# Kernel tuning notes

Measured on AMD Instinct MI355X. Metric: run time of the kernel, lower is better.

Reference implementation:

```python
import jax, jax.numpy as jnp
import numpy as np

V = 50257       # vocab size (leaves of Huffman tree)
N_DEC = V - 1   # internal decision nodes
D = 1024        # input_size
N_EX = 8192     # number of examples (tokens)
MAX_LEN = 24    # max Huffman path depth


def setup_inputs() -> dict:
    key = jax.random.key(0)
    k_x, k_w, k_t, k_p, k_c, k_l = jax.random.split(key, 6)
    x = jax.random.normal(k_x, (N_EX, D), dtype=jnp.float32)
    W = jax.random.normal(k_w, (N_DEC, D), dtype=jnp.float32) * 0.02
    t = jax.random.randint(k_t, (N_EX,), 0, V, dtype=jnp.int32)
    # padded per-leaf tree paths: decision-node indices and +/-1 branch codes
    paths = jax.random.randint(k_p, (V, MAX_LEN), 0, N_DEC, dtype=jnp.int32)
    codes = jnp.where(jax.random.bernoulli(k_c, 0.5, (V, MAX_LEN)), 1.0, -1.0).astype(jnp.float32)
    lens = jax.random.randint(k_l, (V,), 1, MAX_LEN + 1, dtype=jnp.int32)
    return {"x": x, "W": W, "t": t, "paths": paths, "codes": codes, "lens": lens}


def reference(x, W, t, paths, codes, lens):
    # Per-example tree path: gather the decision nodes / codes for each target leaf.
    node_idx = paths[t]            # [N_EX, MAX_LEN] int32
    code = codes[t]                # [N_EX, MAX_LEN] +/-1
    mask = (jnp.arange(MAX_LEN)[None, :] < lens[t][:, None]).astype(x.dtype)  # [N_EX, MAX_LEN]
    # Irregular gather of W rows along each path, then per-step dot products.
    Wp = W[node_idx]               # [N_EX, MAX_LEN, D]
    wxy = code * jnp.einsum('nd,nld->nl', x, Wp)   # [N_EX, MAX_LEN]
    # Per-decision binary log-loss: log(1 + exp(-wxy)), masked to true path length.
    ls = jax.nn.softplus(-wxy) * mask
    return ls.sum()
```

## Files before the change

kernel.cpp:

```cpp
#include <hip/hip_runtime.h>
#include <math.h>

#define HS_D       1024
#define HS_MAXLEN  24
#define HS_PAIRS   12
#define HS_NBUCKET 512

__global__ __launch_bounds__(256) void hsm_pair_kernel(
    const float* __restrict__ x,
    const float* __restrict__ W,
    const int*   __restrict__ t,
    const int*   __restrict__ paths,
    const float* __restrict__ codes,
    const int*   __restrict__ lens,
    float*       __restrict__ ws,
    int n_ex)
{
    const int tid  = threadIdx.x;
    const int lane = tid & 63;
    const int gw   = blockIdx.x * 4 + (tid >> 6);
    const int n    = gw / HS_PAIRS;
    const int p    = gw % HS_PAIRS;

    const int leaf = t[n];
    const int L    = lens[leaf];
    const int l0   = 2 * p;
    const int l1   = l0 + 1;
    if (l0 >= L) return;

    const int   node0 = paths[leaf * HS_MAXLEN + l0];
    const float c0    = codes[leaf * HS_MAXLEN + l0];
    const bool  v1    = (l1 < L);
    const int   node1 = v1 ? paths[leaf * HS_MAXLEN + l1] : node0;
    const float c1    = v1 ? codes[leaf * HS_MAXLEN + l1] : 1.0f;

    const float4* x4 = (const float4*)(x + (size_t)n     * HS_D);
    const float4* w0 = (const float4*)(W + (size_t)node0 * HS_D);
    const float4* w1 = (const float4*)(W + (size_t)node1 * HS_D);

    float4 xf[4], wf0[4], wf1[4];
#pragma unroll
    for (int j = 0; j < 4; ++j) xf[j]  = x4[j * 64 + lane];
#pragma unroll
    for (int j = 0; j < 4; ++j) wf0[j] = w0[j * 64 + lane];
#pragma unroll
    for (int j = 0; j < 4; ++j) wf1[j] = w1[j * 64 + lane];

    float d0 = 0.0f, d1 = 0.0f;
#pragma unroll
    for (int j = 0; j < 4; ++j) {
        d0 += xf[j].x * wf0[j].x + xf[j].y * wf0[j].y
            + xf[j].z * wf0[j].z + xf[j].w * wf0[j].w;
        d1 += xf[j].x * wf1[j].x + xf[j].y * wf1[j].y
            + xf[j].z * wf1[j].z + xf[j].w * wf1[j].w;
    }

#pragma unroll
    for (int off = 32; off > 0; off >>= 1) {
        d0 += __shfl_down(d0, off);
        d1 += __shfl_down(d1, off);
    }

    if (lane == 0) {
        const float z0 = -c0 * d0;
        float v = fmaxf(z0, 0.0f) + log1pf(expf(-fabsf(z0)));
        if (v1) {
            const float z1 = -c1 * d1;
            v += fmaxf(z1, 0.0f) + log1pf(expf(-fabsf(z1)));
        }
        atomicAdd(&ws[gw & (HS_NBUCKET - 1)], v);
    }
}

__global__ __launch_bounds__(64) void hsm_finish_kernel(
    const float* __restrict__ ws, float* __restrict__ out)
{
    const int lane = threadIdx.x;
    float s = 0.0f;
#pragma unroll
    for (int k = 0; k < HS_NBUCKET / 64; ++k)
        s += ws[lane + 64 * k];
#pragma unroll
    for (int off = 32; off > 0; off >>= 1)
        s += __shfl_down(s, off);
    if (lane == 0) out[0] = s;
}

extern "C" void kernel_launch(void* const* d_in, const int* in_sizes, int n_in,
                              void* d_out, int out_size, void* d_ws, size_t ws_size,
                              hipStream_t stream) {
    const float* x     = (const float*)d_in[0];
    const float* W     = (const float*)d_in[1];
    const int*   t     = (const int*)  d_in[2];
    const int*   paths = (const int*)  d_in[3];
    const float* codes = (const float*)d_in[4];
    const int*   lens  = (const int*)  d_in[5];
    float* out = (float*)d_out;
    float* ws  = (float*)d_ws;

    const int n_ex = in_sizes[2];

    hipMemsetAsync(ws, 0, HS_NBUCKET * sizeof(float), stream);

    const int n_waves  = n_ex * HS_PAIRS;
    const int n_blocks = (n_waves + 3) / 4;
    hsm_pair_kernel<<<n_blocks, 256, 0, stream>>>(x, W, t, paths, codes, lens,
                                                  ws, n_ex);
    hsm_finish_kernel<<<1, 64, 0, stream>>>(ws, out);
}
```

Baseline: 324.2 us.

## Warm L2/MALL with a streaming prefetch pass and drop atomic bucket reduction

```diff
diff --git a/kernel.cpp b/kernel.cpp
--- a/kernel.cpp
+++ b/kernel.cpp
@@ -4,7 +4,26 @@
 #define HS_D       1024
 #define HS_MAXLEN  24
 #define HS_PAIRS   12
-#define HS_NBUCKET 512
+#define HS_PF_OFF  (1u << 21)
+
+__global__ __launch_bounds__(256) void hsm_prefetch_kernel(
+    const float4* __restrict__ W4, int nW4,
+    const float4* __restrict__ x4, int nx4,
+    float* __restrict__ ws)
+{
+    const int tid    = blockIdx.x * blockDim.x + threadIdx.x;
+    const int stride = gridDim.x * blockDim.x;
+    float s = 0.0f;
+    for (int i = tid; i < nW4; i += stride) {
+        const float4 v = W4[i];
+        s += v.x + v.y + v.z + v.w;
+    }
+    for (int i = tid; i < nx4; i += stride) {
+        const float4 v = x4[i];
+        s += v.x + v.y + v.z + v.w;
+    }
+    ws[HS_PF_OFF + tid] = s;
+}
 
 __global__ __launch_bounds__(256) void hsm_pair_kernel(
     const float* __restrict__ x,
@@ -13,8 +32,7 @@
     const int*   __restrict__ paths,
     const float* __restrict__ codes,
     const int*   __restrict__ lens,
-    float*       __restrict__ ws,
-    int n_ex)
+    float*       __restrict__ ws)
 {
     const int tid  = threadIdx.x;
     const int lane = tid & 63;
@@ -26,7 +44,10 @@
     const int L    = lens[leaf];
     const int l0   = 2 * p;
     const int l1   = l0 + 1;
-    if (l0 >= L) return;
+    if (l0 >= L) {
+        if (lane == 0) ws[gw] = 0.0f;
+        return;
+    }
 
     const int   node0 = paths[leaf * HS_MAXLEN + l0];
     const float c0    = codes[leaf * HS_MAXLEN + l0];
@@ -34,17 +55,17 @@
     const int   node1 = v1 ? paths[leaf * HS_MAXLEN + l1] : node0;
     const float c1    = v1 ? codes[leaf * HS_MAXLEN + l1] : 1.0f;
 
-    const float4* x4 = (const float4*)(x + (size_t)n     * HS_D);
     const float4* w0 = (const float4*)(W + (size_t)node0 * HS_D);
     const float4* w1 = (const float4*)(W + (size_t)node1 * HS_D);
+    const float4* x4 = (const float4*)(x + (size_t)n     * HS_D);
 
-    float4 xf[4], wf0[4], wf1[4];
-#pragma unroll
-    for (int j = 0; j < 4; ++j) xf[j]  = x4[j * 64 + lane];
+    float4 wf0[4], wf1[4], xf[4];
 #pragma unroll
     for (int j = 0; j < 4; ++j) wf0[j] = w0[j * 64 + lane];
 #pragma unroll
     for (int j = 0; j < 4; ++j) wf1[j] = w1[j * 64 + lane];
+#pragma unroll
+    for (int j = 0; j < 4; ++j) xf[j]  = x4[j * 64 + lane];
 
     float d0 = 0.0f, d1 = 0.0f;
 #pragma unroll
@@ -68,22 +89,29 @@
             const float z1 = -c1 * d1;
             v += fmaxf(z1, 0.0f) + log1pf(expf(-fabsf(z1)));
         }
-        atomicAdd(&ws[gw & (HS_NBUCKET - 1)], v);
+        ws[gw] = v;
     }
 }
 
-__global__ __launch_bounds__(64) void hsm_finish_kernel(
-    const float* __restrict__ ws, float* __restrict__ out)
+__global__ __launch_bounds__(1024) void hsm_finish_kernel(
+    const float* __restrict__ ws, int n_slots, float* __restrict__ out)
 {
-    const int lane = threadIdx.x;
+    const int tid = threadIdx.x;
     float s = 0.0f;
-#pragma unroll
-    for (int k = 0; k < HS_NBUCKET / 64; ++k)
-        s += ws[lane + 64 * k];
+    for (int i = tid; i < n_slots; i += 1024)
+        s += ws[i];
 #pragma unroll
     for (int off = 32; off > 0; off >>= 1)
         s += __shfl_down(s, off);
-    if (lane == 0) out[0] = s;
+    __shared__ float sred[16];
+    if ((tid & 63) == 0) sred[tid >> 6] = s;
+    __syncthreads();
+    if (tid == 0) {
+        float tot = 0.0f;
+#pragma unroll
+        for (int w = 0; w < 16; ++w) tot += sred[w];
+        out[0] = tot;
+    }
 }
 
 extern "C" void kernel_launch(void* const* d_in, const int* in_sizes, int n_in,
@@ -99,12 +127,15 @@
     float* ws  = (float*)d_ws;
 
     const int n_ex = in_sizes[2];
+    const int nW4  = in_sizes[1] / 4;
+    const int nx4  = in_sizes[0] / 4;
 
-    hipMemsetAsync(ws, 0, HS_NBUCKET * sizeof(float), stream);
+    hsm_prefetch_kernel<<<4096, 256, 0, stream>>>(
+        (const float4*)W, nW4, (const float4*)x, nx4, ws);
 
     const int n_waves  = n_ex * HS_PAIRS;
     const int n_blocks = (n_waves + 3) / 4;
-    hsm_pair_kernel<<<n_blocks, 256, 0, stream>>>(x, W, t, paths, codes, lens,
-                                                  ws, n_ex);
-    hsm_finish_kernel<<<1, 64, 0, stream>>>(ws, out);
+    hsm_pair_kernel<<<n_blocks, 256, 0, stream>>>(x, W, t, paths, codes, lens, ws);
+
+    hsm_finish_kernel<<<1, 1024, 0, stream>>>(ws, n_waves, out);
 }
```

After: 397.2 us. 22.5% more time.
